# Kernel tuning notes

Hardware: AMD Instinct MI355X
Metric: run time of the kernel (lower is better)

The kernel has to match this reference:

```python
import jax, jax.numpy as jnp
import numpy as np

D_IN = 128
D_H = 128
N_CHILD = 8
BATCH = 32768


def setup_inputs() -> dict:
    key = jax.random.key(0)
    ks = jax.random.split(key, 16)
    stdev = 1.0 / np.sqrt(D_H)

    def unif(k, shape):
        return jax.random.uniform(k, shape, jnp.float32, -stdev, stdev)

    inp = {
        "x": jax.random.normal(ks[0], (BATCH, D_IN), jnp.float32),
        "h": jax.random.normal(ks[1], (N_CHILD, BATCH, D_H), jnp.float32),
        "C": jax.random.normal(ks[2], (N_CHILD, BATCH, D_H), jnp.float32),
        "W_i": unif(ks[3], (D_IN, D_H)),
        "W_f": unif(ks[4], (D_IN, D_H)),
        "W_o": unif(ks[5], (D_IN, D_H)),
        "W_u": unif(ks[6], (D_IN, D_H)),
        "U_i": unif(ks[7], (D_H, D_H)),
        "U_f": unif(ks[8], (D_H, D_H)),
        "U_o": unif(ks[9], (D_H, D_H)),
        "U_u": unif(ks[10], (D_H, D_H)),
        "b_i": unif(ks[11], (1, D_H)),
        "b_f": unif(ks[12], (1, D_H)),
        "b_o": unif(ks[13], (1, D_H)),
        "b_u": unif(ks[14], (1, D_H)),
    }
    return inp


def reference(x, h, C, W_i, W_f, W_o, W_u, U_i, U_f, U_o, U_u, b_i, b_f, b_o, b_u):
    # x: [B, D_in]; h, C: [N_child, B, H]
    h_tilde = jnp.sum(h, axis=0)  # [B, H]
    i_j = jax.nn.sigmoid(x @ W_i + h_tilde @ U_i + b_i)  # [B, H]
    o_j = jax.nn.sigmoid(x @ W_o + h_tilde @ U_o + b_o)  # [B, H]
    f_x = x @ W_f  # [B, H]
    # per-child forget gates, vectorized over the child axis
    f_j = jax.nn.sigmoid(f_x[None] + jnp.einsum('nbh,hk->nbk', h, U_f) + b_f)  # [N, B, H]
    u_j = jnp.tanh(x @ W_u + h_tilde @ U_u + b_u)  # [B, H]
    c_j = i_j * u_j + jnp.sum(f_j * C, axis=0)  # [B, H]
    h_j = o_j * jnp.tanh(c_j)
    return (h_j, c_j)
```

## Files before the change

### kernel.cpp

```cpp
#include <hip/hip_runtime.h>

#define NB 32768
#define NCH 8
#define ROWS 32

#define WAITL0 asm volatile("s_waitcnt lgkmcnt(0)" ::: "memory")

typedef __bf16 bf16x8 __attribute__((ext_vector_type(8)));
typedef float f32x4 __attribute__((ext_vector_type(4)));
typedef unsigned int u32;
typedef unsigned short u16;
typedef u32 u32x4v __attribute__((ext_vector_type(4)));
typedef u32 u32x2v __attribute__((ext_vector_type(2)));

__device__ __align__(16) u16 g_wt[8 * 128 * 128];

__device__ __forceinline__ u16 f2bf(float f) {
  u32 u = __builtin_bit_cast(u32, f);
  u32 r = u + 0x7FFFu + ((u >> 16) & 1u);
  return (u16)(r >> 16);
}
__device__ __forceinline__ float bf2f(u16 b) {
  u32 u = (u32)b << 16;
  return __builtin_bit_cast(float, u);
}
__device__ __forceinline__ float sigm(float s) {
  return __builtin_amdgcn_rcpf(1.0f + __expf(-s));
}
__device__ __forceinline__ float tanh_f(float v) {
  float e = __expf(2.0f * v);
  return 1.0f - 2.0f * __builtin_amdgcn_rcpf(e + 1.0f);
}

__global__ void prep_weights(const float* __restrict__ Wi, const float* __restrict__ Wf,
                             const float* __restrict__ Wo, const float* __restrict__ Wu,
                             const float* __restrict__ Ui, const float* __restrict__ Uf,
                             const float* __restrict__ Uo, const float* __restrict__ Uu) {
  __shared__ float t[128][129];
  const float* srcs[8] = {Wi, Wf, Wo, Wu, Ui, Uf, Uo, Uu};
  const float* s = srcs[blockIdx.x];
  for (int i = threadIdx.x; i < 16384; i += 256) t[i >> 7][i & 127] = s[i];
  __syncthreads();
  u16* dst = g_wt + blockIdx.x * 16384;
  for (int i = threadIdx.x; i < 16384; i += 256) {
    int n = i >> 7, k = i & 127;
    dst[i] = f2bf(t[k][n]);
  }
}

__device__ __forceinline__ bf16x8 ldA(const u32x4v* buf, int row, int ks, int g) {
  u32x4v v = buf[row * 16 + ((ks * 4 + g) ^ (row & 7))];
  return __builtin_bit_cast(bf16x8, v);
}
__device__ __forceinline__ bf16x8 ldB(const u16* wt, int col, int ks, int g) {
  return __builtin_bit_cast(bf16x8, *(const u32x4v*)(wt + col * 128 + ks * 32 + g * 8));
}

__device__ __forceinline__ void stage_load(const float* __restrict__ src, int tid, f32x4 v[4]) {
#pragma unroll
  for (int i = 0; i < 4; ++i) {
    int q = tid + (i << 8);
    v[i] = *(const f32x4*)(src + (q >> 5) * 128 + (q & 31) * 4);
  }
}
__device__ __forceinline__ u32x2v pack2(f32x4 v) {
  u32x2v p;
  p[0] = (u32)f2bf(v[0]) | ((u32)f2bf(v[1]) << 16);
  p[1] = (u32)f2bf(v[2]) | ((u32)f2bf(v[3]) << 16);
  return p;
}
__device__ __forceinline__ void stage_write(u32x4v* buf, int tid, const f32x4 v[4]) {
  u32x2v* b2 = (u32x2v*)buf;
#pragma unroll
  for (int i = 0; i < 4; ++i) {
    int q = tid + (i << 8);
    int r = q >> 5, c4 = q & 31;
    b2[r * 32 + (c4 ^ ((r & 7) << 1))] = pack2(v[i]);
  }
}

__device__ __forceinline__ void commit_tiles(u32x4v* hdst, u16* cdst, int tid,
                                             const f32x4 hv[4], const f32x4 cv[4],
                                             f32x4 htacc[4]) {
  u32x2v* hb2 = (u32x2v*)hdst;
  u32x2v* cb2 = (u32x2v*)cdst;
#pragma unroll
  for (int i = 0; i < 4; ++i) {
    int q = tid + (i << 8);
    int r = q >> 5, c4 = q & 31;
    htacc[i] += hv[i];
    hb2[r * 32 + (c4 ^ ((r & 7) << 1))] = pack2(hv[i]);
    cb2[r * 32 + (c4 ^ (((r >> 2) & 3) << 2))] = pack2(cv[i]);
  }
}

__device__ __forceinline__ void gemm_g(const u32x4v* a, const u16* wt, int cl, int g,
                                       int cb, f32x4 acc[2][2]) {
#pragma unroll
  for (int ks = 0; ks < 4; ++ks) {
    bf16x8 b0 = ldB(wt, cb + cl, ks, g);
    bf16x8 b1 = ldB(wt, cb + 16 + cl, ks, g);
    bf16x8 a0 = ldA(a, cl, ks, g);
    bf16x8 a1 = ldA(a, 16 + cl, ks, g);
    acc[0][0] = __builtin_amdgcn_mfma_f32_16x16x32_bf16(a0, b0, acc[0][0], 0, 0, 0);
    acc[0][1] = __builtin_amdgcn_mfma_f32_16x16x32_bf16(a0, b1, acc[0][1], 0, 0, 0);
    acc[1][0] = __builtin_amdgcn_mfma_f32_16x16x32_bf16(a1, b0, acc[1][0], 0, 0, 0);
    acc[1][1] = __builtin_amdgcn_mfma_f32_16x16x32_bf16(a1, b1, acc[1][1], 0, 0, 0);
  }
}

__device__ __forceinline__ int fxsw(int row, int dw) {
  int k = (row >> 2) & 3;
  return row * 128 + (dw ^ (((k & 1) << 4) | ((k >> 1) << 2)));
}
__device__ __forceinline__ void exch(float* ex, const f32x4 fr[2][2], int g, int cl,
                                     int cb, int tid, f32x4 s4[4]) {
  __syncthreads();
#pragma unroll
  for (int m = 0; m < 2; ++m)
#pragma unroll
    for (int nf = 0; nf < 2; ++nf) {
      int col = cb + nf * 16 + cl;
#pragma unroll
      for (int r_ = 0; r_ < 4; ++r_)
        ex[fxsw(m * 16 + g * 4 + r_, col)] = fr[m][nf][r_];
    }
  __syncthreads();
  int sr = tid >> 5, sc = (tid & 31) * 4;
#pragma unroll
  for (int i = 0; i < 4; ++i)
    s4[i] = *(const f32x4*)(ex + fxsw(sr + i * 8, sc));
}

__device__ __forceinline__ void child_compute(const u32x4v* hcur, const u16* ccur,
                                              const bf16x8 uf0[4], const bf16x8 uf1[4],
                                              const f32x4 afx[2][2], float bf0, float bf1,
                                              int cl, int g, int cb, f32x4 accc[2][2]) {
  f32x4 f[2][2];
#pragma unroll
  for (int m = 0; m < 2; ++m) { f[m][0] = afx[m][0]; f[m][1] = afx[m][1]; }
#pragma unroll
  for (int ks = 0; ks < 4; ++ks) {
    bf16x8 a0 = ldA(hcur, cl, ks, g);
    bf16x8 a1 = ldA(hcur, 16 + cl, ks, g);
    f[0][0] = __builtin_amdgcn_mfma_f32_16x16x32_bf16(a0, uf0[ks], f[0][0], 0, 0, 0);
    f[0][1] = __builtin_amdgcn_mfma_f32_16x16x32_bf16(a0, uf1[ks], f[0][1], 0, 0, 0);
    f[1][0] = __builtin_amdgcn_mfma_f32_16x16x32_bf16(a1, uf0[ks], f[1][0], 0, 0, 0);
    f[1][1] = __builtin_amdgcn_mfma_f32_16x16x32_bf16(a1, uf1[ks], f[1][1], 0, 0, 0);
  }
#pragma unroll
  for (int m = 0; m < 2; ++m)
#pragma unroll
    for (int nf = 0; nf < 2; ++nf) {
      float bfv = nf ? bf1 : bf0;
#pragma unroll
      for (int r = 0; r < 4; ++r) {
        int row = m * 16 + g * 4 + r;
        int lc = (cb + nf * 16 + cl) ^ (g << 4);
        float cval = bf2f(ccur[row * 128 + lc]);
        accc[m][nf][r] += sigm(f[m][nf][r] + bfv) * cval;
      }
    }
}

__global__ __launch_bounds__(256) void tree_lstm(
    const float* __restrict__ x, const float* __restrict__ h, const float* __restrict__ C,
    const float* __restrict__ b_i, const float* __restrict__ b_f,
    const float* __restrict__ b_o, const float* __restrict__ b_u,
    float* __restrict__ out) {
  __shared__ u32x4v hbf[2][ROWS * 16];
  __shared__ u16 cbf[2][ROWS * 128];
  __shared__ u32x4v xs[ROWS * 16];

  const int tid = threadIdx.x;
  const int lane = tid & 63;
  const int wv = tid >> 6;
  const int cb = wv * 32;
  const int row0 = blockIdx.x * ROWS;
  const int g = lane >> 4;
  const int cl = lane & 15;
  const int sr = tid >> 5;
  const int sc = (tid & 31) * 4;
  const f32x4 fz = {0.f, 0.f, 0.f, 0.f};

  f32x4 xv[4];
  stage_load(x + (size_t)row0 * 128, tid, xv);
  const float bf0 = b_f[cb + cl], bf1 = b_f[cb + 16 + cl];
  const float bi0 = b_i[cb + cl], bi1 = b_i[cb + 16 + cl];
  const float bo0 = b_o[cb + cl], bo1 = b_o[cb + 16 + cl];
  const float bu0 = b_u[cb + cl], bu1 = b_u[cb + 16 + cl];

  stage_write(xs, tid, xv);
  __syncthreads();

  f32x4 hv[4], cv[4];
  stage_load(h + (size_t)row0 * 128, tid, hv);
  stage_load(C + (size_t)row0 * 128, tid, cv);
  __builtin_amdgcn_sched_barrier(0);

  bf16x8 uf0[4], uf1[4];
#pragma unroll
  for (int ks = 0; ks < 4; ++ks) {
    uf0[ks] = ldB(g_wt + 5 * 16384, cb + cl, ks, g);
    uf1[ks] = ldB(g_wt + 5 * 16384, cb + 16 + cl, ks, g);
  }
  f32x4 afx[2][2];
#pragma unroll
  for (int m = 0; m < 2; ++m) { afx[m][0] = fz; afx[m][1] = fz; }
  gemm_g(xs, g_wt + 1 * 16384, cl, g, cb, afx);

  f32x4 accc[2][2];
#pragma unroll
  for (int m = 0; m < 2; ++m) { accc[m][0] = fz; accc[m][1] = fz; }
  f32x4 htacc[4] = {fz, fz, fz, fz};

  commit_tiles(hbf[0], cbf[0], tid, hv, cv, htacc);
  stage_load(h + ((size_t)NB + row0) * 128, tid, hv);
  stage_load(C + ((size_t)NB + row0) * 128, tid, cv);
  __builtin_amdgcn_sched_barrier(0);
  WAITL0;
  __builtin_amdgcn_s_barrier();

#pragma unroll 1
  for (int n = 0; n < NCH - 1; ++n) {
    child_compute(hbf[n & 1], cbf[n & 1], uf0, uf1, afx, bf0, bf1, cl, g, cb, accc);

    commit_tiles(hbf[(n + 1) & 1], cbf[(n + 1) & 1], tid, hv, cv, htacc);
    if (n < NCH - 2) {
      stage_load(h + ((size_t)(n + 2) * NB + row0) * 128, tid, hv);
      stage_load(C + ((size_t)(n + 2) * NB + row0) * 128, tid, cv);
      __builtin_amdgcn_sched_barrier(0);
    }
    WAITL0;
    __builtin_amdgcn_s_barrier();
  }

  child_compute(hbf[1], cbf[1], uf0, uf1, afx, bf0, bf1, cl, g, cb, accc);
  __syncthreads();

  stage_write(hbf[0], tid, htacc);
  __syncthreads();
  const u32x4v* ht = hbf[0];
  float* ex = (float*)cbf;

  f32x4 pre[2][2], s4[4];

#pragma unroll
  for (int m = 0; m < 2; ++m) { pre[m][0] = fz; pre[m][1] = fz; }
  gemm_g(xs, g_wt + 3 * 16384, cl, g, cb, pre);
  gemm_g(ht, g_wt + 7 * 16384, cl, g, cb, pre);
  f32x4 uF[2][2];
#pragma unroll
  for (int m = 0; m < 2; ++m)
#pragma unroll
    for (int nf = 0; nf < 2; ++nf) {
      float bv = nf ? bu1 : bu0;
#pragma unroll
      for (int r = 0; r < 4; ++r) uF[m][nf][r] = tanh_f(pre[m][nf][r] + bv);
    }

#pragma unroll
  for (int m = 0; m < 2; ++m) { pre[m][0] = fz; pre[m][1] = fz; }
  gemm_g(xs, g_wt + 0 * 16384, cl, g, cb, pre);
  gemm_g(ht, g_wt + 4 * 16384, cl, g, cb, pre);
  f32x4 cF[2][2], tF[2][2];
#pragma unroll
  for (int m = 0; m < 2; ++m)
#pragma unroll
    for (int nf = 0; nf < 2; ++nf) {
      float bv = nf ? bi1 : bi0;
#pragma unroll
      for (int r = 0; r < 4; ++r) {
        float cv2 = sigm(pre[m][nf][r] + bv) * uF[m][nf][r] + accc[m][nf][r];
        cF[m][nf][r] = cv2;
        tF[m][nf][r] = tanh_f(cv2);
      }
    }
  exch(ex, cF, g, cl, cb, tid, s4);
  float* outc = out + (size_t)NB * 128;
#pragma unroll
  for (int i = 0; i < 4; ++i)
    *(f32x4*)(outc + (size_t)(row0 + sr + i * 8) * 128 + sc) = s4[i];

#pragma unroll
  for (int m = 0; m < 2; ++m) { pre[m][0] = fz; pre[m][1] = fz; }
  gemm_g(xs, g_wt + 2 * 16384, cl, g, cb, pre);
  gemm_g(ht, g_wt + 6 * 16384, cl, g, cb, pre);
  f32x4 hF[2][2];
#pragma unroll
  for (int m = 0; m < 2; ++m)
#pragma unroll
    for (int nf = 0; nf < 2; ++nf) {
      float bv = nf ? bo1 : bo0;
#pragma unroll
      for (int r = 0; r < 4; ++r)
        hF[m][nf][r] = sigm(pre[m][nf][r] + bv) * tF[m][nf][r];
    }
  exch(ex, hF, g, cl, cb, tid, s4);
#pragma unroll
  for (int i = 0; i < 4; ++i)
    *(f32x4*)(out + (size_t)(row0 + sr + i * 8) * 128 + sc) = s4[i];
}

extern "C" void kernel_launch(void* const* d_in, const int* in_sizes, int n_in,
                              void* d_out, int out_size, void* d_ws, size_t ws_size,
                              hipStream_t stream) {
  (void)in_sizes; (void)n_in; (void)out_size; (void)d_ws; (void)ws_size;
  const float* x = (const float*)d_in[0];
  const float* h = (const float*)d_in[1];
  const float* C = (const float*)d_in[2];

  prep_weights<<<8, 256, 0, stream>>>(
      (const float*)d_in[3], (const float*)d_in[4], (const float*)d_in[5],
      (const float*)d_in[6], (const float*)d_in[7], (const float*)d_in[8],
      (const float*)d_in[9], (const float*)d_in[10]);

  tree_lstm<<<NB / ROWS, 256, 0, stream>>>(
      x, h, C,
      (const float*)d_in[11], (const float*)d_in[12],
      (const float*)d_in[13], (const float*)d_in[14],
      (float*)d_out);
}
```

Measured before the change: 108.3 us.

## Load C directly into MFMA fragment layout and shrink LDS footprint

C tiles are no longer staged through shared memory as bf16. Each lane now loads its MFMA accumulator-layout elements straight from global memory in fp32, which removes the C LDS writes and reads and a bf16 rounding step. U_f is reloaded from the weight buffer on every child iteration instead of being held in registers, which frees registers at the cost of extra weight reads. The output exchange now goes through a 16-bit LDS buffer, so final outputs are rounded to bf16 and precision drops. The direct C loads are scalar and strided, so memory coalescing gets worse.

```diff
diff --git a/kernel.cpp b/kernel.cpp
--- a/kernel.cpp
+++ b/kernel.cpp
@@ -20,8 +20,8 @@
   u32 r = u + 0x7FFFu + ((u >> 16) & 1u);
   return (u16)(r >> 16);
 }
-__device__ __forceinline__ float bf2f(u16 b) {
-  u32 u = (u32)b << 16;
+__device__ __forceinline__ float bf2f(u32 b) {
+  u32 u = b << 16;
   return __builtin_bit_cast(float, u);
 }
 __device__ __forceinline__ float sigm(float s) {
@@ -79,19 +79,28 @@
   }
 }
 
-__device__ __forceinline__ void commit_tiles(u32x4v* hdst, u16* cdst, int tid,
-                                             const f32x4 hv[4], const f32x4 cv[4],
-                                             f32x4 htacc[4]) {
+__device__ __forceinline__ void commit_h(u32x4v* hdst, int tid, const f32x4 hv[4],
+                                         f32x4 htacc[4]) {
   u32x2v* hb2 = (u32x2v*)hdst;
-  u32x2v* cb2 = (u32x2v*)cdst;
 #pragma unroll
   for (int i = 0; i < 4; ++i) {
     int q = tid + (i << 8);
     int r = q >> 5, c4 = q & 31;
     htacc[i] += hv[i];
     hb2[r * 32 + (c4 ^ ((r & 7) << 1))] = pack2(hv[i]);
-    cb2[r * 32 + (c4 ^ (((r >> 2) & 3) << 2))] = pack2(cv[i]);
-  }
+  }
+}
+
+__device__ __forceinline__ void loadC_frag(const float* __restrict__ Cn, int g, int cl,
+                                           int cb, f32x4 cfr[2][2]) {
+#pragma unroll
+  for (int m = 0; m < 2; ++m)
+#pragma unroll
+    for (int nf = 0; nf < 2; ++nf) {
+      const float* p = Cn + (m * 16 + g * 4) * 128 + cb + nf * 16 + cl;
+#pragma unroll
+      for (int r = 0; r < 4; ++r) cfr[m][nf][r] = p[r * 128];
+    }
 }
 
 __device__ __forceinline__ void gemm_g(const u32x4v* a, const u16* wt, int cl, int g,
@@ -109,12 +118,8 @@
   }
 }
 
-__device__ __forceinline__ int fxsw(int row, int dw) {
-  int k = (row >> 2) & 3;
-  return row * 128 + (dw ^ (((k & 1) << 4) | ((k >> 1) << 2)));
-}
-__device__ __forceinline__ void exch(float* ex, const f32x4 fr[2][2], int g, int cl,
-                                     int cb, int tid, f32x4 s4[4]) {
+__device__ __forceinline__ void exch16b(u16* ex, const f32x4 fr[2][2], int g, int cl,
+                                        int cb, int tid, f32x4 s4[4]) {
   __syncthreads();
 #pragma unroll
   for (int m = 0; m < 2; ++m)
@@ -123,44 +128,20 @@
       int col = cb + nf * 16 + cl;
 #pragma unroll
       for (int r_ = 0; r_ < 4; ++r_)
-        ex[fxsw(m * 16 + g * 4 + r_, col)] = fr[m][nf][r_];
-    }
-  __syncthreads();
-  int sr = tid >> 5, sc = (tid & 31) * 4;
-#pragma unroll
-  for (int i = 0; i < 4; ++i)
-    s4[i] = *(const f32x4*)(ex + fxsw(sr + i * 8, sc));
-}
-
-__device__ __forceinline__ void child_compute(const u32x4v* hcur, const u16* ccur,
-                                              const bf16x8 uf0[4], const bf16x8 uf1[4],
-                                              const f32x4 afx[2][2], float bf0, float bf1,
-                                              int cl, int g, int cb, f32x4 accc[2][2]) {
-  f32x4 f[2][2];
-#pragma unroll
-  for (int m = 0; m < 2; ++m) { f[m][0] = afx[m][0]; f[m][1] = afx[m][1]; }
-#pragma unroll
-  for (int ks = 0; ks < 4; ++ks) {
-    bf16x8 a0 = ldA(hcur, cl, ks, g);
-    bf16x8 a1 = ldA(hcur, 16 + cl, ks, g);
-    f[0][0] = __builtin_amdgcn_mfma_f32_16x16x32_bf16(a0, uf0[ks], f[0][0], 0, 0, 0);
-    f[0][1] = __builtin_amdgcn_mfma_f32_16x16x32_bf16(a0, uf1[ks], f[0][1], 0, 0, 0);
-    f[1][0] = __builtin_amdgcn_mfma_f32_16x16x32_bf16(a1, uf0[ks], f[1][0], 0, 0, 0);
-    f[1][1] = __builtin_amdgcn_mfma_f32_16x16x32_bf16(a1, uf1[ks], f[1][1], 0, 0, 0);
-  }
-#pragma unroll
-  for (int m = 0; m < 2; ++m)
-#pragma unroll
-    for (int nf = 0; nf < 2; ++nf) {
-      float bfv = nf ? bf1 : bf0;
-#pragma unroll
-      for (int r = 0; r < 4; ++r) {
-        int row = m * 16 + g * 4 + r;
-        int lc = (cb + nf * 16 + cl) ^ (g << 4);
-        float cval = bf2f(ccur[row * 128 + lc]);
-        accc[m][nf][r] += sigm(f[m][nf][r] + bfv) * cval;
-      }
-    }
+        ex[(m * 16 + g * 4 + r_) * 128 + (col ^ (g << 4))] = f2bf(fr[m][nf][r_]);
+    }
+  __syncthreads();
+  const u32x2v* e2 = (const u32x2v*)ex;
+  int sr = tid >> 5, c4 = tid & 31;
+#pragma unroll
+  for (int i = 0; i < 4; ++i) {
+    int row = sr + i * 8;
+    u32x2v p = e2[row * 32 + (c4 ^ (((row >> 2) & 3) << 2))];
+    s4[i][0] = bf2f(p[0] & 0xffffu);
+    s4[i][1] = bf2f(p[0] >> 16);
+    s4[i][2] = bf2f(p[1] & 0xffffu);
+    s4[i][3] = bf2f(p[1] >> 16);
+  }
 }
 
 __global__ __launch_bounds__(256) void tree_lstm(
@@ -169,8 +150,8 @@
     const float* __restrict__ b_o, const float* __restrict__ b_u,
     float* __restrict__ out) {
   __shared__ u32x4v hbf[2][ROWS * 16];
-  __shared__ u16 cbf[2][ROWS * 128];
   __shared__ u32x4v xs[ROWS * 16];
+  __shared__ u16 exb[ROWS * 128];
 
   const int tid = threadIdx.x;
   const int lane = tid & 63;
@@ -193,17 +174,10 @@
   stage_write(xs, tid, xv);
   __syncthreads();
 
-  f32x4 hv[4], cv[4];
+  f32x4 hv[4];
   stage_load(h + (size_t)row0 * 128, tid, hv);
-  stage_load(C + (size_t)row0 * 128, tid, cv);
   __builtin_amdgcn_sched_barrier(0);
 
-  bf16x8 uf0[4], uf1[4];
-#pragma unroll
-  for (int ks = 0; ks < 4; ++ks) {
-    uf0[ks] = ldB(g_wt + 5 * 16384, cb + cl, ks, g);
-    uf1[ks] = ldB(g_wt + 5 * 16384, cb + 16 + cl, ks, g);
-  }
   f32x4 afx[2][2];
 #pragma unroll
   for (int m = 0; m < 2; ++m) { afx[m][0] = fz; afx[m][1] = fz; }
@@ -214,34 +188,46 @@
   for (int m = 0; m < 2; ++m) { accc[m][0] = fz; accc[m][1] = fz; }
   f32x4 htacc[4] = {fz, fz, fz, fz};
 
-  commit_tiles(hbf[0], cbf[0], tid, hv, cv, htacc);
+  commit_h(hbf[0], tid, hv, htacc);
   stage_load(h + ((size_t)NB + row0) * 128, tid, hv);
-  stage_load(C + ((size_t)NB + row0) * 128, tid, cv);
   __builtin_amdgcn_sched_barrier(0);
   WAITL0;
   __builtin_amdgcn_s_barrier();
 
 #pragma unroll 1
-  for (int n = 0; n < NCH - 1; ++n) {
-    child_compute(hbf[n & 1], cbf[n & 1], uf0, uf1, afx, bf0, bf1, cl, g, cb, accc);
-
-    commit_tiles(hbf[(n + 1) & 1], cbf[(n + 1) & 1], tid, hv, cv, htacc);
-    if (n < NCH - 2) {
+  for (int n = 0; n < NCH; ++n) {
+    if (n + 1 < NCH)
+      commit_h(hbf[(n + 1) & 1], tid, hv, htacc);
+
+    f32x4 cfr[2][2];
+    loadC_frag(C + ((size_t)n * NB + row0) * 128, g, cl, cb, cfr);
+    if (n + 2 < NCH)
       stage_load(h + ((size_t)(n + 2) * NB + row0) * 128, tid, hv);
-      stage_load(C + ((size_t)(n + 2) * NB + row0) * 128, tid, cv);
-      __builtin_amdgcn_sched_barrier(0);
-    }
+    __builtin_amdgcn_sched_barrier(0);
+
+    f32x4 f[2][2];
+#pragma unroll
+    for (int m = 0; m < 2; ++m) { f[m][0] = afx[m][0]; f[m][1] = afx[m][1]; }
+    gemm_g(hbf[n & 1], g_wt + 5 * 16384, cl, g, cb, f);
+
+#pragma unroll
+    for (int m = 0; m < 2; ++m)
+#pragma unroll
+      for (int nf = 0; nf < 2; ++nf) {
+        float bfv = nf ? bf1 : bf0;
+#pragma unroll
+        for (int r = 0; r < 4; ++r)
+          accc[m][nf][r] += sigm(f[m][nf][r] + bfv) * cfr[m][nf][r];
+      }
+
     WAITL0;
     __builtin_amdgcn_s_barrier();
   }
-
-  child_compute(hbf[1], cbf[1], uf0, uf1, afx, bf0, bf1, cl, g, cb, accc);
   __syncthreads();
 
   stage_write(hbf[0], tid, htacc);
   __syncthreads();
   const u32x4v* ht = hbf[0];
-  float* ex = (float*)cbf;
 
   f32x4 pre[2][2], s4[4];
 
@@ -276,7 +262,7 @@
         tF[m][nf][r] = tanh_f(cv2);
       }
     }
-  exch(ex, cF, g, cl, cb, tid, s4);
+  exch16b(exb, cF, g, cl, cb, tid, s4);
   float* outc = out + (size_t)NB * 128;
 #pragma unroll
   for (int i = 0; i < 4; ++i)
@@ -296,7 +282,7 @@
       for (int r = 0; r < 4; ++r)
         hF[m][nf][r] = sigm(pre[m][nf][r] + bv) * tF[m][nf][r];
     }
-  exch(ex, hF, g, cl, cb, tid, s4);
+  exch16b(exb, hF, g, cl, cb, tid, s4);
 #pragma unroll
   for (int i = 0; i < 4; ++i)
     *(f32x4*)(out + (size_t)(row0 + sr + i * 8) * 128 + sc) = s4[i];
```

Measured after the change: 134.8 us, median of 3. 24.5% more time.
